# Kernel tuning notes

Measured on AMD Instinct MI355X. Metric: run time of the kernel, lower is better.

The kernel has to match this reference:

```python
import jax, jax.numpy as jnp
import numpy as np

L, N, E, H, D, F = 2048, 2, 1024, 16, 64, 4096  # seq, batch, embed, heads, head_dim, ffn
EPS = 1e-5


def _ln(x, w, b):
    m = jnp.mean(x, axis=-1, keepdims=True)
    v = jnp.mean(jnp.square(x - m), axis=-1, keepdims=True)
    return (x - m) * jax.lax.rsqrt(v + EPS) * w + b


def setup_inputs() -> dict:
    key = jax.random.key(0)
    ks = jax.random.split(key, 16)
    s = 0.02
    f32 = jnp.float32
    return {
        "x": jax.random.normal(ks[0], (L, N, E), f32),
        "ln1_w": jnp.ones((E,), f32),
        "ln1_b": jnp.zeros((E,), f32),
        "wq": jax.random.normal(ks[1], (H * D, E), f32) * s,
        "bq": jnp.zeros((H * D,), f32),
        "wk": jax.random.normal(ks[2], (H * D, E), f32) * s,
        "bk": jnp.zeros((H * D,), f32),
        "wv": jax.random.normal(ks[3], (H * D, E), f32) * s,
        "bv": jnp.zeros((H * D,), f32),
        "wout": jax.random.normal(ks[4], (E, H * D), f32) * s,
        "bout": jnp.zeros((E,), f32),
        "ln2_w": jnp.ones((E,), f32),
        "ln2_b": jnp.zeros((E,), f32),
        "fc1_w": jax.random.normal(ks[5], (F, E), f32) * s,
        "fc1_b": jnp.zeros((F,), f32),
        "fc2_w": jax.random.normal(ks[6], (E, F), f32) * s,
        "fc2_b": jnp.zeros((E,), f32),
    }


def reference(x, ln1_w, ln1_b, wq, bq, wk, bk, wv, bv, wout, bout,
              ln2_w, ln2_b, fc1_w, fc1_b, fc2_w, fc2_b):
    scale = D ** (-0.5)
    residual = x
    h = _ln(x, ln1_w, ln1_b)                      # (L,N,E)
    q = (h @ wq.T + bq).reshape(L, N, H, D) * scale
    k = (h @ wk.T + bk).reshape(L, N, H, D)
    v = (h @ wv.T + bv).reshape(L, N, H, D)
    attn = jnp.einsum('qnhd,knhd->nhqk', q, k)    # (N,H,L,L) full score matrix
    causal = jnp.tril(jnp.ones((L, L), bool))
    attn = jnp.where(causal[None, None], attn, jnp.float32(-10000.0))
    p = jax.nn.softmax(attn, axis=-1)
    o = jnp.einsum('nhqk,knhd->qnhd', p, v).reshape(L, N, H * D)
    o = o @ wout.T + bout
    x = o + residual
    residual = x
    h = _ln(x, ln2_w, ln2_b)
    h = jax.nn.gelu(h @ fc1_w.T + fc1_b, approximate=False)
    h = h @ fc2_w.T + fc2_b
    return h + residual
```

## Files before the change

### kernel.cpp

```cpp
#include <hip/hip_runtime.h>
#include <hip/hip_bf16.h>
#include <math.h>

using bf16 = __hip_bfloat16;
typedef __bf16 bf16x8 __attribute__((ext_vector_type(8)));
typedef short  short4v __attribute__((ext_vector_type(4)));
typedef float  f32x4  __attribute__((ext_vector_type(4)));

static constexpr int Lq = 2048, Nb = 2, E = 1024, Hh = 16, Dd = 64, Ff = 4096;
static constexpr int MT = Lq * Nb;
static constexpr int QKLD = 2 * E;
static constexpr int LDL = 2 * QKLD;

__device__ __forceinline__ void async_lds16(const void* g, void* l) {
  __builtin_amdgcn_global_load_lds(
      (const __attribute__((address_space(1))) void*)g,
      (__attribute__((address_space(3))) void*)l, 16, 0, 0);
}
__device__ __forceinline__ bf16x8 ld8(const bf16* p) { return *(const bf16x8*)p; }
__device__ __forceinline__ short bfbits(float x) {
  bf16 t = __float2bfloat16(x);
  return *(short*)&t;
}
__device__ __forceinline__ float gelu_fast(float v) {
  const float y = fminf(2.302208f * (v + 0.044715f * v * v * v), 80.f);
  const float t = exp2f(y);
  return v * t / (t + 1.0f);
}

__global__ __launch_bounds__(256) void cvt_all_kernel(
    const float* __restrict__ wq, const float* __restrict__ wk,
    const float* __restrict__ wv, const float* __restrict__ wout,
    const float* __restrict__ fc1w, const float* __restrict__ fc2w,
    bf16* __restrict__ wqkvb, bf16* __restrict__ woutb,
    bf16* __restrict__ f1wb, bf16* __restrict__ f2wb) {
  const int i = blockIdx.x * 256 + threadIdx.x;
  const float* src;
  bf16* dst;
  size_t off;
  if (i < 786432) {
    const int r = i >> 18;
    off = (size_t)(i & 262143);
    src = (r == 0) ? wq : (r == 1) ? wk : wv;
    dst = wqkvb + (size_t)r * (E * E);
  } else if (i < 1048576) {
    off = (size_t)(i - 786432); src = wout; dst = woutb;
  } else if (i < 2097152) {
    off = (size_t)(i - 1048576); src = fc1w; dst = f1wb;
  } else {
    off = (size_t)(i - 2097152); src = fc2w; dst = f2wb;
  }
  float4 v = ((const float4*)src)[off];
  bf16 o4[4] = {__float2bfloat16(v.x), __float2bfloat16(v.y),
                __float2bfloat16(v.z), __float2bfloat16(v.w)};
  *(uint2*)(dst + 4 * off) = *(uint2*)o4;
}

template <int EPI, int BK>
__global__ __launch_bounds__(256) void gemm_bt(
    const bf16* __restrict__ A, const bf16* __restrict__ W,
    const float* __restrict__ b1, const float* __restrict__ b2,
    const float* __restrict__ b3, int Klen, int Kstride, int Nld,
    float qscale, int scut, bf16* __restrict__ outb,
    bf16* __restrict__ outv) {
  __shared__ __align__(16) bf16 As[128 * BK];
  __shared__ __align__(16) bf16 Bs[128 * BK];
  const int tid = threadIdx.x;
  const int w = tid >> 6, lane = tid & 63;
  const int quad = lane >> 4, l16 = lane & 15;
  const int wm = (w >> 1) * 64, wn = (w & 1) * 64;
  const int m0 = blockIdx.y * 128, n0 = blockIdx.x * 128;
  const int koff = blockIdx.z * Klen;

  f32x4 acc[4][4];
#pragma unroll
  for (int i = 0; i < 4; i++)
#pragma unroll
    for (int j = 0; j < 4; j++)
#pragma unroll
      for (int r = 0; r < 4; r++) acc[i][j][r] = 0.f;

  if constexpr (BK == 32) {
    const int c0 = w * 64 + lane;
    const int c1 = c0 + 256;
    const size_t arow0 = (size_t)(m0 + (c0 >> 2)), arow1 = (size_t)(m0 + (c1 >> 2));
    const size_t brow0 = (size_t)(n0 + (c0 >> 2)), brow1 = (size_t)(n0 + (c1 >> 2));
    const int col0 = (c0 & 3) * 8, col1 = (c1 & 3) * 8;
    bf16* ldsA0 = &As[(w * 64) * 8];
    bf16* ldsA1 = &As[(256 + w * 64) * 8];
    bf16* ldsB0 = &Bs[(w * 64) * 8];
    bf16* ldsB1 = &Bs[(256 + w * 64) * 8];

    const int nk = Klen >> 5;
    for (int kt = 0; kt < nk; ++kt) {
      const int k0 = koff + kt * 32;
      async_lds16(A + arow0 * Kstride + k0 + col0, ldsA0);
      async_lds16(A + arow1 * Kstride + k0 + col1, ldsA1);
      async_lds16(W + brow0 * Kstride + k0 + col0, ldsB0);
      async_lds16(W + brow1 * Kstride + k0 + col1, ldsB1);
      __syncthreads();
      bf16x8 a[4], b[4];
#pragma unroll
      for (int i = 0; i < 4; i++) {
        a[i] = ld8(&As[(wm + i * 16 + l16) * 32 + quad * 8]);
        b[i] = ld8(&Bs[(wn + i * 16 + l16) * 32 + quad * 8]);
      }
#pragma unroll
      for (int i = 0; i < 4; i++)
#pragma unroll
        for (int j = 0; j < 4; j++)
          acc[i][j] = __builtin_amdgcn_mfma_f32_16x16x32_bf16(a[i], b[j], acc[i][j], 0, 0, 0);
      __syncthreads();
    }
  } else {
    const int rowoff = w * 8 + (lane >> 3);
    const int colsw = (((lane & 7) ^ (lane >> 3)) << 3);

    const int nk = Klen >> 6;
    for (int kt = 0; kt < nk; ++kt) {
      const int k0 = koff + (kt << 6);
#pragma unroll
      for (int r = 0; r < 4; r++) {
        async_lds16(A + (size_t)(m0 + r * 32 + rowoff) * Kstride + k0 + colsw,
                    As + (size_t)(r * 256 + w * 64) * 8);
        async_lds16(W + (size_t)(n0 + r * 32 + rowoff) * Kstride + k0 + colsw,
                    Bs + (size_t)(r * 256 + w * 64) * 8);
      }
      __syncthreads();
#pragma unroll
      for (int ksub = 0; ksub < 2; ksub++) {
        const int gx = ksub * 4 + quad;
        bf16x8 a[4], b[4];
#pragma unroll
        for (int i = 0; i < 4; i++) {
          const int ra = wm + i * 16 + l16;
          const int rb = wn + i * 16 + l16;
          a[i] = ld8(&As[(size_t)(ra * 8 + (gx ^ (l16 & 7))) * 8]);
          b[i] = ld8(&Bs[(size_t)(rb * 8 + (gx ^ (l16 & 7))) * 8]);
        }
#pragma unroll
        for (int i = 0; i < 4; i++)
#pragma unroll
          for (int j = 0; j < 4; j++)
            acc[i][j] = __builtin_amdgcn_mfma_f32_16x16x32_bf16(a[i], b[j], acc[i][j], 0, 0, 0);
      }
      __syncthreads();
    }
  }

  const size_t zoff = (EPI == 3) ? (size_t)blockIdx.z * ((size_t)MT * E) : 0;
#pragma unroll
  for (int i = 0; i < 4; i++) {
    const int mrow = m0 + wm + i * 16 + quad * 4;
#pragma unroll
    for (int j = 0; j < 4; j++) {
      const int ncol = n0 + wn + j * 16 + l16;
      float bv = 0.f;
      if constexpr (EPI != 3) {
        if (b3 != nullptr) {
          bv = (ncol < 1024) ? b1[ncol]
               : (ncol < 2048) ? b2[ncol - 1024] : b3[ncol - 2048];
        } else {
          bv = b1[ncol];
        }
      }
      const float sc = (ncol < scut) ? qscale : 1.0f;
#pragma unroll
      for (int r = 0; r < 4; r++) {
        float v = (acc[i][j][r] + bv) * sc;
        if constexpr (EPI == 2) {
          outb[(size_t)(mrow + r) * Nld + ncol] = __float2bfloat16(gelu_fast(v));
        } else if constexpr (EPI == 3) {
          outb[zoff + (size_t)(mrow + r) * Nld + ncol] = __float2bfloat16(v);
        } else {
          if (ncol < 2048) {
            outb[(size_t)(mrow + r) * 2048 + ncol] = __float2bfloat16(v);
          } else {
            const int h = (ncol - 2048) >> 6, d = ncol & 63;
            const int tok = mrow + r, n = tok & 1, l = tok >> 1;
            outv[(size_t)((n * 16 + h) * 64 + d) * Lq + l] = __float2bfloat16(v);
          }
        }
      }
    }
  }
}

__global__ __launch_bounds__(256) void reduce2_kernel(
    const bf16* __restrict__ P, const float* __restrict__ bias,
    const float* __restrict__ res, float* __restrict__ out) {
  const int i = blockIdx.x * 256 + threadIdx.x;
  const size_t e0 = (size_t)i * 4;
  const int col = (int)(e0 & (E - 1));
  uint2 u0 = *(const uint2*)(P + e0);
  uint2 u1 = *(const uint2*)(P + (size_t)MT * E + e0);
  const bf16* p0 = (const bf16*)&u0;
  const bf16* p1 = (const bf16*)&u1;
  float4 b = *(const float4*)(bias + col);
  float4 r = *(const float4*)(res + e0);
  float4 o;
  o.x = (float)p0[0] + (float)p1[0] + b.x + r.x;
  o.y = (float)p0[1] + (float)p1[1] + b.y + r.y;
  o.z = (float)p0[2] + (float)p1[2] + b.z + r.z;
  o.w = (float)p0[3] + (float)p1[3] + b.w + r.w;
  *(float4*)(out + e0) = o;
}

__global__ __launch_bounds__(256) void redln_kernel(
    const bf16* __restrict__ P, const float* __restrict__ bias,
    const float* __restrict__ res, const float* __restrict__ wgt,
    const float* __restrict__ bia, float* __restrict__ x1,
    bf16* __restrict__ h2) {
  const int t = blockIdx.x, tid = threadIdx.x;
  const size_t base = (size_t)t * E;
  const int e0 = tid * 4;
  uint2 u0 = *(const uint2*)(P + base + e0);
  uint2 u1 = *(const uint2*)(P + (size_t)MT * E + base + e0);
  const bf16* p0 = (const bf16*)&u0;
  const bf16* p1 = (const bf16*)&u1;
  float4 b = *(const float4*)(bias + e0);
  float4 r = *(const float4*)(res + base + e0);
  float v4[4];
  v4[0] = (float)p0[0] + (float)p1[0] + b.x + r.x;
  v4[1] = (float)p0[1] + (float)p1[1] + b.y + r.y;
  v4[2] = (float)p0[2] + (float)p1[2] + b.z + r.z;
  v4[3] = (float)p0[3] + (float)p1[3] + b.w + r.w;
  *(float4*)(x1 + base + e0) = *(float4*)v4;

  float s = 0.f, ss = 0.f;
#pragma unroll
  for (int i = 0; i < 4; i++) { s += v4[i]; ss += v4[i] * v4[i]; }
  for (int off = 32; off > 0; off >>= 1) {
    s += __shfl_down(s, off, 64);
    ss += __shfl_down(ss, off, 64);
  }
  __shared__ float rs[4], rss[4], mv[2];
  const int w = tid >> 6;
  if ((tid & 63) == 0) { rs[w] = s; rss[w] = ss; }
  __syncthreads();
  if (tid == 0) {
    float S = rs[0] + rs[1] + rs[2] + rs[3];
    float SS = rss[0] + rss[1] + rss[2] + rss[3];
    float mean = S * (1.f / E);
    float var = SS * (1.f / E) - mean * mean;
    mv[0] = mean; mv[1] = rsqrtf(var + 1e-5f);
  }
  __syncthreads();
  const float mean = mv[0], rstd = mv[1];
  float4 wg = *(const float4*)(wgt + e0);
  float4 bb = *(const float4*)(bia + e0);
  bf16 o4[4];
  o4[0] = __float2bfloat16((v4[0] - mean) * rstd * wg.x + bb.x);
  o4[1] = __float2bfloat16((v4[1] - mean) * rstd * wg.y + bb.y);
  o4[2] = __float2bfloat16((v4[2] - mean) * rstd * wg.z + bb.z);
  o4[3] = __float2bfloat16((v4[3] - mean) * rstd * wg.w + bb.w);
  *(uint2*)(h2 + base + e0) = *(uint2*)o4;
}

__global__ __launch_bounds__(256) void ln_kernel(
    const float* __restrict__ x, const float* __restrict__ wgt,
    const float* __restrict__ bia, bf16* __restrict__ out) {
  const int t = blockIdx.x, tid = threadIdx.x;
  const size_t base = (size_t)t * E;
  float v4[4], s = 0.f, ss = 0.f;
#pragma unroll
  for (int i = 0; i < 4; i++) {
    float v = x[base + i * 256 + tid];
    v4[i] = v; s += v; ss += v * v;
  }
  for (int off = 32; off > 0; off >>= 1) {
    s += __shfl_down(s, off, 64);
    ss += __shfl_down(ss, off, 64);
  }
  __shared__ float rs[4], rss[4], mv[2];
  const int w = tid >> 6;
  if ((tid & 63) == 0) { rs[w] = s; rss[w] = ss; }
  __syncthreads();
  if (tid == 0) {
    float S = rs[0] + rs[1] + rs[2] + rs[3];
    float SS = rss[0] + rss[1] + rss[2] + rss[3];
    float mean = S * (1.f / E);
    float var = SS * (1.f / E) - mean * mean;
    mv[0] = mean; mv[1] = rsqrtf(var + 1e-5f);
  }
  __syncthreads();
  const float mean = mv[0], rstd = mv[1];
#pragma unroll
  for (int i = 0; i < 4; i++) {
    const int e = i * 256 + tid;
    float r = (v4[i] - mean) * rstd * wgt[e] + bia[e];
    out[base + e] = __float2bfloat16(r);
  }
}

__global__ __launch_bounds__(256) void attn_kernel(
    const bf16* __restrict__ QK, const bf16* __restrict__ VT,
    bf16* __restrict__ O) {
  __shared__ __align__(16) bf16 KB[512 * 8];
  __shared__ __align__(16) bf16 VB[512 * 8];
  const int tid = threadIdx.x;
  const int w = tid >> 6, lane = tid & 63, quad = lane >> 4, l16 = lane & 15;
  const int bid = blockIdx.x;
  const int x = bid & 7;
  const int m = (bid >> 3) & 31;
  const int g = bid >> 8;
  const int j = m >> 2;
  const int hh = (m & 3) * 8 + x;
  const int qt = (g == 0) ? j : (g == 1) ? (31 - j) : (g == 2) ? (j + 8) : (23 - j);
  const int n = hh >> 4, h = hh & 15;

  const bf16* Qp = QK + n * QKLD + h * Dd;
  const bf16* Kp = Qp + E;
  const bf16* Vp = VT + (size_t)hh * 64 * Lq;

  bf16* ldsK0 = KB + (size_t)(w * 64) * 8;
  bf16* ldsK1 = KB + (size_t)(256 + w * 64) * 8;
  bf16* ldsV0 = VB + (size_t)(w * 64) * 8;
  bf16* ldsV1 = VB + (size_t)(256 + w * 64) * 8;
  const int w8 = w * 8;

  const int ql = qt * 64 + w * 16 + l16;
  const bf16x8 aq0 = ld8(Qp + (size_t)ql * LDL + quad * 8);
  const bf16x8 aq1 = ld8(Qp + (size_t)ql * LDL + 32 + quad * 8);

  f32x4 o_acc[4];
#pragma unroll
  for (int d = 0; d < 4; d++)
#pragma unroll
    for (int r = 0; r < 4; r++) o_acc[d][r] = 0.f;
  float m_run = -3e30f, l_run = 0.f;

  for (int kt = 0; kt <= qt; ++kt) {
    const size_t kb = (size_t)kt * 64;

    async_lds16(Kp + (size_t)(kb + lane) * LDL + w8, ldsK0);
    async_lds16(Kp + (size_t)(kb + lane) * LDL + 32 + w8, ldsK1);
    async_lds16(Vp + (size_t)lane * Lq + kb + w8, ldsV0);
    async_lds16(Vp + (size_t)lane * Lq + kb + 32 + w8, ldsV1);
    __syncthreads();

    f32x4 s[4];
#pragma unroll
    for (int ks = 0; ks < 4; ks++) {
      const bf16x8 kc0 = ld8(&KB[(size_t)((quad)*64 + ks * 16 + l16) * 8]);
      const bf16x8 kc1 = ld8(&KB[(size_t)((4 + quad) * 64 + ks * 16 + l16) * 8]);
#pragma unroll
      for (int r = 0; r < 4; r++) s[ks][r] = 0.f;
      s[ks] = __builtin_amdgcn_mfma_f32_16x16x32_bf16(kc0, aq0, s[ks], 0, 0, 0);
      s[ks] = __builtin_amdgcn_mfma_f32_16x16x32_bf16(kc1, aq1, s[ks], 0, 0, 0);
    }

    if (kt == qt) {
#pragma unroll
      for (int ks = 0; ks < 4; ks++) {
#pragma unroll
        for (int r = 0; r < 4; r++) {
          const int kg = kt * 64 + ks * 16 + quad * 4 + r;
          if (kg > ql) s[ks][r] = -14427.0f;
        }
      }
    }

    float tmax = s[0][0];
#pragma unroll
    for (int ks = 0; ks < 4; ks++)
#pragma unroll
      for (int r = 0; r < 4; r++) tmax = fmaxf(tmax, s[ks][r]);
    tmax = fmaxf(tmax, __shfl_xor(tmax, 16, 64));
    tmax = fmaxf(tmax, __shfl_xor(tmax, 32, 64));
    const float mnew = fmaxf(m_run, tmax);
    const float alpha = exp2f(m_run - mnew);
    m_run = mnew;
    float rsum = 0.f;
    short4v pf[4];
#pragma unroll
    for (int ks = 0; ks < 4; ks++) {
#pragma unroll
      for (int r = 0; r < 4; r++) {
        const float pv = exp2f(s[ks][r] - mnew);
        rsum += pv;
        pf[ks][r] = bfbits(pv);
      }
    }
    rsum += __shfl_xor(rsum, 16, 64);
    rsum += __shfl_xor(rsum, 32, 64);
    l_run = l_run * alpha + rsum;
#pragma unroll
    for (int d = 0; d < 4; d++)
#pragma unroll
      for (int r = 0; r < 4; r++) o_acc[d][r] *= alpha;

#pragma unroll
    for (int d = 0; d < 4; d++) {
#pragma unroll
      for (int ks = 0; ks < 4; ks++) {
        const int gg = ks * 2 + (quad >> 1);
        const short4v av =
            *(const short4v*)&VB[(size_t)(gg * 64 + d * 16 + l16) * 8 + (quad & 1) * 4];
        o_acc[d] = __builtin_amdgcn_mfma_f32_16x16x16bf16_1k(av, pf[ks], o_acc[d], 0, 0, 0);
      }
    }
    __syncthreads();
  }

  const float inv_l = 1.f / fmaxf(l_run, 1e-30f);
  const size_t obase = (size_t)ql * (Nb * E) + (size_t)n * E + h * Dd;
#pragma unroll
  for (int d = 0; d < 4; d++)
#pragma unroll
    for (int r = 0; r < 4; r++)
      O[obase + d * 16 + quad * 4 + r] = __float2bfloat16(o_acc[d][r] * inv_l);
}

extern "C" void kernel_launch(void* const* d_in, const int* in_sizes, int n_in,
                              void* d_out, int out_size, void* d_ws, size_t ws_size,
                              hipStream_t stream) {
  const float* x    = (const float*)d_in[0];
  const float* ln1w = (const float*)d_in[1];
  const float* ln1b = (const float*)d_in[2];
  const float* wq   = (const float*)d_in[3];
  const float* bq   = (const float*)d_in[4];
  const float* wk   = (const float*)d_in[5];
  const float* bk   = (const float*)d_in[6];
  const float* wv   = (const float*)d_in[7];
  const float* bv   = (const float*)d_in[8];
  const float* wout = (const float*)d_in[9];
  const float* bout = (const float*)d_in[10];
  const float* ln2w = (const float*)d_in[11];
  const float* ln2b = (const float*)d_in[12];
  const float* fc1w = (const float*)d_in[13];
  const float* fc1b = (const float*)d_in[14];
  const float* fc2w = (const float*)d_in[15];
  const float* fc2b = (const float*)d_in[16];

  char* ws = (char*)d_ws;
  bf16* wqkvb = (bf16*)(ws);
  bf16* woutb = (bf16*)(ws + ((size_t)6 << 20));
  bf16* f1wb  = (bf16*)(ws + ((size_t)8 << 20));
  bf16* f2wb  = (bf16*)(ws + ((size_t)16 << 20));
  bf16* h1    = (bf16*)(ws + ((size_t)24 << 20));
  bf16* qk    = (bf16*)(ws + ((size_t)32 << 20));
  bf16* vtg   = (bf16*)(ws + ((size_t)48 << 20));
  bf16* o     = (bf16*)(ws + ((size_t)56 << 20));
  float* x1   = (float*)(ws + ((size_t)64 << 20));
  bf16* Pout  = (bf16*)(ws + ((size_t)32 << 20));
  bf16* P01   = (bf16*)(ws);
  bf16* f1    = (bf16*)(ws + ((size_t)32 << 20));
  bf16* h2    = h1;
  float* outp = (float*)d_out;

  cvt_all_kernel<<<12288, 256, 0, stream>>>(wq, wk, wv, wout, fc1w, fc2w,
                                            wqkvb, woutb, f1wb, f2wb);

  ln_kernel<<<MT, 256, 0, stream>>>(x, ln1w, ln1b, h1);

  dim3 gQKV(3 * E / 128, MT / 128);
  dim3 gE2(E / 128, MT / 128, 2);
  dim3 gF(Ff / 128, MT / 128);

  gemm_bt<4, 64><<<gQKV, 256, 0, stream>>>(h1, wqkvb, bq, bk, bv, E, E, 2048,
                                           0.125f * 1.44269504f, 1024, qk, vtg);

  attn_kernel<<<1024, 256, 0, stream>>>(qk, vtg, o);

  gemm_bt<3, 64><<<gE2, 256, 0, stream>>>(o, woutb, nullptr, nullptr, nullptr,
                                          E / 2, E, E, 1.f, 0, Pout, nullptr);
  redln_kernel<<<MT, 256, 0, stream>>>(Pout, bout, x, ln2w, ln2b, x1, h2);

  gemm_bt<2, 32><<<gF, 256, 0, stream>>>(h2, f1wb, fc1b, nullptr, nullptr,
                                         E, E, Ff, 1.f, 0, f1, nullptr);

  gemm_bt<3, 64><<<gE2, 256, 0, stream>>>(f1, f2wb, nullptr, nullptr, nullptr,
                                          Ff / 2, Ff, E, 1.f, 0, P01, nullptr);
  reduce2_kernel<<<MT * E / 1024, 256, 0, stream>>>(P01, fc2b, x1, outp);
}
```

Baseline: 396.5 us.

## Use 256x256-tile 8-wave pipelined GEMM for FC1+GELU

Replaces the 128x128-tile FC1 GEMM with a new 512-thread kernel that computes 256x256 output tiles using double-buffered async global-to-LDS loads split into four interleaved phases, with barriers and priority hints around the MFMA blocks. The larger tile raises arithmetic intensity and cuts global and LDS traffic per FLOP. The trade-offs are 128KB of dynamic LDS and heavy register use, and only 16x16=256 blocks for the 256 CUs, which risks wave quantization and lower occupancy. The epilogue writes bf16 directly with non-coalesced per-element stores.

Measured after the change: 375.5 us. 1.06x faster.

```diff
diff --git a/kernel.cpp b/kernel.cpp
--- a/kernel.cpp
+++ b/kernel.cpp
@@ -186,6 +186,202 @@
   }
 }
 
+template <int S, int H>
+__device__ __forceinline__ void load_frags256(const char* Ab, const char* Bb,
+                                              const int (&aoff)[8], const int (&boff)[4],
+                                              bf16x8 (&a)[4], bf16x8 (&b)[4]) {
+#pragma unroll
+  for (int i = 0; i < 4; i++) a[i] = ld8((const bf16*)(Ab + S * 16384 + aoff[H * 4 + i]));
+#pragma unroll
+  for (int j = 0; j < 4; j++) b[j] = ld8((const bf16*)(Bb + S * 16384 + boff[j]));
+}
+
+template <int H>
+__device__ __forceinline__ void mfma256(const bf16x8 (&a)[4], const bf16x8 (&b)[4],
+                                        f32x4 (&acc)[8][4]) {
+#pragma unroll
+  for (int i = 0; i < 4; i++)
+#pragma unroll
+    for (int j = 0; j < 4; j++)
+      acc[H * 4 + i][j] =
+          __builtin_amdgcn_mfma_f32_16x16x32_bf16(a[i], b[j], acc[H * 4 + i][j], 0, 0, 0);
+}
+
+template <int K, int NOUT>
+__global__ __launch_bounds__(512, 2) void gemm256_gelu(
+    const bf16* __restrict__ A, const bf16* __restrict__ W,
+    const float* __restrict__ bias, bf16* __restrict__ out) {
+  extern __shared__ char smem[];
+  constexpr int NKT = K / 64;
+  static_assert(NKT >= 2, "need >=2 K-tiles");
+  const int tid = threadIdx.x;
+  const int w = tid >> 6, lane = tid & 63;
+  const int quad = lane >> 4, l16 = lane & 15;
+  const int wr = w >> 2, wc = w & 3;
+  const int m0 = blockIdx.y * 256, n0 = blockIdx.x * 256;
+
+  const int o0 = tid << 4;
+  const int o1 = o0 + 8192;
+  const int r0 = o0 >> 6, r1 = o1 >> 6;
+  const int c0 = ((((o0 >> 4) & 3) ^ ((o0 >> 7) & 3)) << 3);
+  const int c1 = ((((o1 >> 4) & 3) ^ ((o1 >> 7) & 3)) << 3);
+  const bf16* Ag0 = A + (size_t)(m0 + r0) * K + c0;
+  const bf16* Ag1 = A + (size_t)(m0 + r1) * K + c1;
+  const bf16* Wg0 = W + (size_t)(n0 + r0) * K + c0;
+  const bf16* Wg1 = W + (size_t)(n0 + r1) * K + c1;
+  const int ldsw = w << 10;
+
+  int aoff[8], boff[4];
+#pragma unroll
+  for (int h = 0; h < 2; h++)
+#pragma unroll
+    for (int i = 0; i < 4; i++) {
+      const int ra = wr * 128 + h * 64 + i * 16 + l16;
+      aoff[h * 4 + i] = ra * 64 + ((quad ^ ((ra >> 1) & 3)) << 4);
+    }
+#pragma unroll
+  for (int j = 0; j < 4; j++) {
+    const int rb = wc * 64 + j * 16 + l16;
+    boff[j] = rb * 64 + ((quad ^ ((rb >> 1) & 3)) << 4);
+  }
+
+  f32x4 acc[8][4];
+#pragma unroll
+  for (int i = 0; i < 8; i++)
+#pragma unroll
+    for (int j = 0; j < 4; j++)
+#pragma unroll
+      for (int r = 0; r < 4; r++) acc[i][j][r] = 0.f;
+
+  {
+    char* d = smem;
+    async_lds16(Ag0, d + ldsw);
+    async_lds16(Ag1, d + 8192 + ldsw);
+    async_lds16(Wg0, d + 32768 + ldsw);
+    async_lds16(Wg1, d + 32768 + 8192 + ldsw);
+    async_lds16(Ag0 + 32, d + 16384 + ldsw);
+    async_lds16(Ag1 + 32, d + 16384 + 8192 + ldsw);
+    async_lds16(Wg0 + 32, d + 49152 + ldsw);
+    async_lds16(Wg1 + 32, d + 49152 + 8192 + ldsw);
+  }
+  asm volatile("s_waitcnt vmcnt(4)" ::: "memory");
+  __builtin_amdgcn_s_barrier();
+
+  for (int kt = 0; kt < NKT; ++kt) {
+    const char* Ab = smem + ((kt & 1) << 16);
+    const char* Bb = Ab + 32768;
+    char* Sd = smem + (((kt + 1) & 1) << 16);
+    const int kn = (kt + 1) << 6;
+    if (kt + 1 < NKT) {
+      {
+        bf16x8 a[4], b[4];
+        load_frags256<0, 0>(Ab, Bb, aoff, boff, a, b);
+        async_lds16(Ag0 + kn, Sd + ldsw);
+        async_lds16(Ag1 + kn, Sd + 8192 + ldsw);
+        __builtin_amdgcn_s_barrier();
+        __builtin_amdgcn_s_setprio(1);
+        mfma256<0>(a, b, acc);
+        __builtin_amdgcn_s_setprio(0);
+        __builtin_amdgcn_sched_barrier(0);
+        __builtin_amdgcn_s_barrier();
+      }
+      {
+        bf16x8 a[4], b[4];
+        load_frags256<0, 1>(Ab, Bb, aoff, boff, a, b);
+        async_lds16(Wg0 + kn, Sd + 32768 + ldsw);
+        async_lds16(Wg1 + kn, Sd + 32768 + 8192 + ldsw);
+        __builtin_amdgcn_s_barrier();
+        __builtin_amdgcn_s_setprio(1);
+        mfma256<1>(a, b, acc);
+        __builtin_amdgcn_s_setprio(0);
+        asm volatile("s_waitcnt vmcnt(4)" ::: "memory");
+        __builtin_amdgcn_sched_barrier(0);
+        __builtin_amdgcn_s_barrier();
+      }
+      {
+        bf16x8 a[4], b[4];
+        load_frags256<1, 0>(Ab, Bb, aoff, boff, a, b);
+        async_lds16(Ag0 + kn + 32, Sd + 16384 + ldsw);
+        async_lds16(Ag1 + kn + 32, Sd + 16384 + 8192 + ldsw);
+        __builtin_amdgcn_s_barrier();
+        __builtin_amdgcn_s_setprio(1);
+        mfma256<0>(a, b, acc);
+        __builtin_amdgcn_s_setprio(0);
+        __builtin_amdgcn_sched_barrier(0);
+        __builtin_amdgcn_s_barrier();
+      }
+      {
+        bf16x8 a[4], b[4];
+        load_frags256<1, 1>(Ab, Bb, aoff, boff, a, b);
+        async_lds16(Wg0 + kn + 32, Sd + 49152 + ldsw);
+        async_lds16(Wg1 + kn + 32, Sd + 49152 + 8192 + ldsw);
+        __builtin_amdgcn_s_barrier();
+        __builtin_amdgcn_s_setprio(1);
+        mfma256<1>(a, b, acc);
+        __builtin_amdgcn_s_setprio(0);
+        asm volatile("s_waitcnt vmcnt(4)" ::: "memory");
+        __builtin_amdgcn_sched_barrier(0);
+        __builtin_amdgcn_s_barrier();
+      }
+    } else {
+      {
+        bf16x8 a[4], b[4];
+        load_frags256<0, 0>(Ab, Bb, aoff, boff, a, b);
+        __builtin_amdgcn_s_barrier();
+        __builtin_amdgcn_s_setprio(1);
+        mfma256<0>(a, b, acc);
+        __builtin_amdgcn_s_setprio(0);
+        __builtin_amdgcn_sched_barrier(0);
+        __builtin_amdgcn_s_barrier();
+      }
+      {
+        bf16x8 a[4], b[4];
+        load_frags256<0, 1>(Ab, Bb, aoff, boff, a, b);
+        __builtin_amdgcn_s_barrier();
+        __builtin_amdgcn_s_setprio(1);
+        mfma256<1>(a, b, acc);
+        __builtin_amdgcn_s_setprio(0);
+        asm volatile("s_waitcnt vmcnt(0)" ::: "memory");
+        __builtin_amdgcn_sched_barrier(0);
+        __builtin_amdgcn_s_barrier();
+      }
+      {
+        bf16x8 a[4], b[4];
+        load_frags256<1, 0>(Ab, Bb, aoff, boff, a, b);
+        __builtin_amdgcn_s_barrier();
+        __builtin_amdgcn_s_setprio(1);
+        mfma256<0>(a, b, acc);
+        __builtin_amdgcn_s_setprio(0);
+        __builtin_amdgcn_sched_barrier(0);
+        __builtin_amdgcn_s_barrier();
+      }
+      {
+        bf16x8 a[4], b[4];
+        load_frags256<1, 1>(Ab, Bb, aoff, boff, a, b);
+        __builtin_amdgcn_s_barrier();
+        __builtin_amdgcn_s_setprio(1);
+        mfma256<1>(a, b, acc);
+        __builtin_amdgcn_s_setprio(0);
+      }
+    }
+  }
+
+#pragma unroll
+  for (int j = 0; j < 4; j++) {
+    const int col = n0 + wc * 64 + j * 16 + l16;
+    const float bv = bias[col];
+#pragma unroll
+    for (int mI = 0; mI < 8; mI++) {
+      const int row = m0 + wr * 128 + mI * 16 + quad * 4;
+#pragma unroll
+      for (int r = 0; r < 4; r++) {
+        out[(size_t)(row + r) * NOUT + col] =
+            __float2bfloat16(gelu_fast(acc[mI][j][r] + bv));
+      }
+    }
+  }
+}
+
 __global__ __launch_bounds__(256) void reduce2_kernel(
     const bf16* __restrict__ P, const float* __restrict__ bias,
     const float* __restrict__ res, float* __restrict__ out) {
@@ -449,6 +645,13 @@
   bf16* h2    = h1;
   float* outp = (float*)d_out;
 
+  static bool g_shmem_attr = false;
+  if (!g_shmem_attr) {
+    hipFuncSetAttribute(reinterpret_cast<const void*>(gemm256_gelu<1024, 4096>),
+                        hipFuncAttributeMaxDynamicSharedMemorySize, 131072);
+    g_shmem_attr = true;
+  }
+
   cvt_all_kernel<<<12288, 256, 0, stream>>>(wq, wk, wv, wout, fc1w, fc2w,
                                             wqkvb, woutb, f1wb, f2wb);
 
@@ -456,7 +659,6 @@
 
   dim3 gQKV(3 * E / 128, MT / 128);
   dim3 gE2(E / 128, MT / 128, 2);
-  dim3 gF(Ff / 128, MT / 128);
 
   gemm_bt<4, 64><<<gQKV, 256, 0, stream>>>(h1, wqkvb, bq, bk, bv, E, E, 2048,
                                            0.125f * 1.44269504f, 1024, qk, vtg);
@@ -467,8 +669,8 @@
                                           E / 2, E, E, 1.f, 0, Pout, nullptr);
   redln_kernel<<<MT, 256, 0, stream>>>(Pout, bout, x, ln2w, ln2b, x1, h2);
 
-  gemm_bt<2, 32><<<gF, 256, 0, stream>>>(h2, f1wb, fc1b, nullptr, nullptr,
-                                         E, E, Ff, 1.f, 0, f1, nullptr);
+  gemm256_gelu<1024, 4096><<<dim3(Ff / 256, MT / 256), 512, 131072, stream>>>(
+      h2, f1wb, fc1b, f1);
 
   gemm_bt<3, 64><<<gE2, 256, 0, stream>>>(f1, f2wb, nullptr, nullptr, nullptr,
                                           Ff / 2, Ff, E, 1.f, 0, P01, nullptr);
```
